# Optimization experiments

Measured on AMD Instinct MI355X. Metric: run time of the kernel, lower is better.

## Reference

```python
import jax, jax.numpy as jnp
import numpy as np
import math

D_MODEL = 1024
N_HEADS = 16
D_HEAD = D_MODEL // N_HEADS
D_FF = 4 * D_MODEL
EPS = 1e-5


def layer_norm(x, gamma, beta):
    mu = jnp.mean(x, axis=-1, keepdims=True)
    var = jnp.var(x, axis=-1, keepdims=True)
    return (x - mu) * jax.lax.rsqrt(var + EPS) * gamma + beta


def setup_inputs() -> dict:
    key = jax.random.key(0)
    ks = jax.random.split(key, 8)
    B, C, D = 32, 256, D_MODEL
    s = 0.02
    return {
        "X": jax.random.normal(ks[0], (B, C, D), dtype=jnp.float32),
        "W_qkv": jax.random.normal(ks[1], (D, 3 * D), dtype=jnp.float32) * s,
        "b_qkv": jnp.zeros((3 * D,), dtype=jnp.float32),
        "W_proj": jax.random.normal(ks[2], (D, D), dtype=jnp.float32) * s,
        "b_proj": jnp.zeros((D,), dtype=jnp.float32),
        "g1": jnp.ones((D,), dtype=jnp.float32),
        "beta1": jnp.zeros((D,), dtype=jnp.float32),
        "g2": jnp.ones((D,), dtype=jnp.float32),
        "beta2": jnp.zeros((D,), dtype=jnp.float32),
        "W_ff1": jax.random.normal(ks[3], (D, D_FF), dtype=jnp.float32) * s,
        "b_ff1": jnp.zeros((D_FF,), dtype=jnp.float32),
        "W_ff2": jax.random.normal(ks[4], (D_FF, D), dtype=jnp.float32) * s,
        "b_ff2": jnp.zeros((D,), dtype=jnp.float32),
    }


def reference(X, W_qkv, b_qkv, W_proj, b_proj, g1, beta1, g2, beta2,
              W_ff1, b_ff1, W_ff2, b_ff2):
    B, C, D = X.shape
    H, Dh = N_HEADS, D_HEAD
    scale = 1.0 / math.sqrt(Dh)

    Xn = layer_norm(X, g1, beta1)
    qkv = Xn @ W_qkv + b_qkv                       # [B, C, 3D]
    q, k, v = jnp.split(qkv, 3, axis=-1)
    # split heads -> [B, H, C, Dh]
    sh = lambda t: t.reshape(B, C, H, Dh).transpose(0, 2, 1, 3)
    q, k, v = sh(q), sh(k), sh(v)

    scores = jnp.einsum("bhcd,bhkd->bhck", q, k) * scale  # [B, H, C, C]
    attn = jax.nn.softmax(scores, axis=-1)
    ctx = jnp.einsum("bhck,bhkd->bhcd", attn, v)           # [B, H, C, Dh]
    ctx = ctx.transpose(0, 2, 1, 3).reshape(B, C, D)

    X1 = X + (ctx @ W_proj + b_proj)
    X2n = layer_norm(X1, g2, beta2)
    h = jax.nn.gelu(X2n @ W_ff1 + b_ff1, approximate=False)
    X_out = X1 + (h @ W_ff2 + b_ff2)
    A = attn.mean(axis=1)                                   # [B, C, C]
    return (X_out, A)
```

## Files before the change

### kernel.cpp

```cpp
#include <hip/hip_runtime.h>
#include <cstdint>
#include <cstddef>

typedef short bf16x8 __attribute__((ext_vector_type(8)));
typedef float f32x4 __attribute__((ext_vector_type(4)));
typedef unsigned short u16;
typedef u16 u16x8 __attribute__((ext_vector_type(8)));

#define GLD16(gptr, lptr)                                                            \
  __builtin_amdgcn_global_load_lds((const __attribute__((address_space(1))) void*)(gptr), \
                                   (__attribute__((address_space(3))) void*)(lptr), 16, 0, 0)

__device__ __forceinline__ u16 f2bf(float f) {
  union { float f; unsigned u; } v; v.f = f;
  unsigned r = v.u + 0x7FFF + ((v.u >> 16) & 1);
  return (u16)(r >> 16);
}
__device__ __forceinline__ float bf2f(u16 h) {
  union { unsigned u; float f; } v; v.u = ((unsigned)h) << 16;
  return v.f;
}

template <int N> __device__ __forceinline__ void vmwait() {
  if constexpr (N == 0) asm volatile("s_waitcnt vmcnt(0)" ::: "memory");
  else if constexpr (N == 6) asm volatile("s_waitcnt vmcnt(6)" ::: "memory");
  else asm volatile("s_waitcnt vmcnt(12)" ::: "memory");
}

__device__ __forceinline__ bf16x8 lds_read_sw64(const u16* base, int row, int col) {
  int byt = row * 128 + col * 2;
  byt ^= (row & 7) << 4;
  return *(const bf16x8*)((const char*)base + byt);
}

__global__ __launch_bounds__(256) void transpose_cast(const float* __restrict__ in,
                                                      u16* __restrict__ out, int R, int C) {
  __shared__ float tile[32][33];
  const int tx = threadIdx.x, ty = threadIdx.y;
  const int c0 = blockIdx.x * 32, r0 = blockIdx.y * 32;
#pragma unroll
  for (int i = 0; i < 32; i += 8)
    tile[ty + i][tx] = in[(size_t)(r0 + ty + i) * C + c0 + tx];
  __syncthreads();
#pragma unroll
  for (int i = 0; i < 32; i += 8)
    out[(size_t)(c0 + ty + i) * R + r0 + tx] = f2bf(tile[tx][ty + i]);
}

__global__ __launch_bounds__(256) void layernorm_bf16(const float* __restrict__ X,
                                                      const float* __restrict__ g,
                                                      const float* __restrict__ be,
                                                      u16* __restrict__ out) {
  const int row = blockIdx.x, t = threadIdx.x;
  const int lane = t & 63, wave = t >> 6;
  const float* x = X + (size_t)row * 1024;
  __shared__ float part[4];
  float v[4]; float s = 0.f;
#pragma unroll
  for (int i = 0; i < 4; ++i) { v[i] = x[t + i * 256]; s += v[i]; }
#pragma unroll
  for (int o = 32; o >= 1; o >>= 1) s += __shfl_xor(s, o);
  if (lane == 0) part[wave] = s;
  __syncthreads();
  const float mu = (part[0] + part[1] + part[2] + part[3]) * (1.f / 1024.f);
  float d2 = 0.f;
#pragma unroll
  for (int i = 0; i < 4; ++i) { float d = v[i] - mu; d2 += d * d; }
#pragma unroll
  for (int o = 32; o >= 1; o >>= 1) d2 += __shfl_xor(d2, o);
  __syncthreads();
  if (lane == 0) part[wave] = d2;
  __syncthreads();
  const float var = (part[0] + part[1] + part[2] + part[3]) * (1.f / 1024.f);
  const float rstd = rsqrtf(var + 1e-5f);
#pragma unroll
  for (int i = 0; i < 4; ++i) {
    const int c = t + i * 256;
    out[(size_t)row * 1024 + c] = f2bf((v[i] - mu) * rstd * g[c] + be[c]);
  }
}

template <int EPI>
__global__ __launch_bounds__(512, 1) void gemm_ring3(const u16* __restrict__ A,
                                                     const u16* __restrict__ Bt,
                                                     const float* __restrict__ bias,
                                                     const float* __restrict__ res,
                                                     float* __restrict__ outf,
                                                     u16* __restrict__ outb,
                                                     int M, int N, int K) {
  constexpr int ABYT = 256 * 128;
  constexpr int BBYT = 128 * 128;
  __shared__ __attribute__((aligned(16))) char lds[3 * (ABYT + BBYT)];

  const int t = threadIdx.x, lane = t & 63, wave = t >> 6;
  const int wm = wave >> 1, wn = wave & 1;
  const int l15 = lane & 15, l16 = lane >> 4;

  const int lb = (blockIdx.x & 7) * ((int)gridDim.x >> 3) + ((int)blockIdx.x >> 3);
  const int NBN = N >> 7;
  const int bm = (lb / NBN) * 256, bn = (lb % NBN) * 128;

  const u16* aptr[4];
  const u16* bptr[2];
#pragma unroll
  for (int c = 0; c < 4; ++c) {
    int Lb = c * 8192 + t * 16;
    int x = (Lb ^ ((Lb >> 3) & 0x70)) >> 1;
    aptr[c] = A + (size_t)(bm + (x >> 6)) * K + (x & 63);
  }
#pragma unroll
  for (int c = 0; c < 2; ++c) {
    int Lb = c * 8192 + t * 16;
    int x = (Lb ^ ((Lb >> 3) & 0x70)) >> 1;
    bptr[c] = Bt + (size_t)(bn + (x >> 6)) * K + (x & 63);
  }

  auto stage = [&](int p) {
    const int ko = p * 64;
    const int s = p % 3;
    char* ab = lds + s * ABYT + t * 16;
    char* bb = lds + 3 * ABYT + s * BBYT + t * 16;
#pragma unroll
    for (int c = 0; c < 4; ++c) GLD16(aptr[c] + ko, ab + c * 8192);
#pragma unroll
    for (int c = 0; c < 2; ++c) GLD16(bptr[c] + ko, bb + c * 8192);
  };
  stage(0); stage(1);

  const int rxA = ((wm * 64 + l15) & 7) << 4;
  const int co0 = l16 * 16, co1 = 64 + l16 * 16;

  f32x4 acc[4][4] = {};
  const int nkt = K >> 6;

#pragma unroll 1
  for (int kt = 0; kt < nkt; ++kt) {
    if (kt < nkt - 1) vmwait<6>(); else vmwait<0>();
    asm volatile("s_barrier" ::: "memory");
    if (kt + 2 < nkt) stage(kt + 2);

    const int s = kt % 3;
    const char* ab = lds + s * ABYT;
    const char* bb = lds + 3 * ABYT + s * BBYT;
    bf16x8 a[4][2], b[4][2];
#pragma unroll
    for (int m = 0; m < 4; ++m) {
      const int r = wm * 64 + m * 16 + l15;
      const int rb = r * 128, sw = (r & 7) << 4;
      a[m][0] = *(const bf16x8*)(ab + rb + (co0 ^ sw));
      a[m][1] = *(const bf16x8*)(ab + rb + (co1 ^ sw));
    }
#pragma unroll
    for (int n = 0; n < 4; ++n) {
      const int r = wn * 64 + n * 16 + l15;
      const int rb = r * 128, sw = (r & 7) << 4;
      b[n][0] = *(const bf16x8*)(bb + rb + (co0 ^ sw));
      b[n][1] = *(const bf16x8*)(bb + rb + (co1 ^ sw));
    }
    __builtin_amdgcn_s_setprio(1);
#pragma unroll
    for (int ks = 0; ks < 2; ++ks)
#pragma unroll
      for (int m = 0; m < 4; ++m)
#pragma unroll
        for (int n = 0; n < 4; ++n)
          acc[m][n] = __builtin_amdgcn_mfma_f32_16x16x32_bf16(a[m][ks], b[n][ks], acc[m][n], 0, 0, 0);
    __builtin_amdgcn_s_setprio(0);
  }

  const int r0 = l16 * 4;
#pragma unroll
  for (int m = 0; m < 4; ++m) {
#pragma unroll
    for (int n = 0; n < 4; ++n) {
      const int col = bn + wn * 64 + n * 16 + l15;
      const float bv = bias[col];
#pragma unroll
      for (int r = 0; r < 4; ++r) {
        const int row = bm + wm * 64 + m * 16 + r0 + r;
        const float v = acc[m][n][r] + bv;
        const size_t o = (size_t)row * N + col;
        if (EPI == 0) {
          outb[o] = f2bf(v);
        } else if (EPI == 1) {
          outf[o] = res[o] + v;
        } else {
          const float u = 0.7978845608f * (v + 0.044715f * v * v * v);
          const float e = __expf(2.f * u);
          const float th = 1.f - 2.f / (1.f + e);
          outb[o] = f2bf(0.5f * v * (1.f + th));
        }
      }
    }
  }
}

__global__ __launch_bounds__(256) void attn_scores(const u16* __restrict__ qkv,
                                                   u16* __restrict__ probs) {
  __shared__ u16 Ks[256 * 64];
  __shared__ u16 Qs[64 * 64];
  const int t = threadIdx.x, lane = t & 63, wave = t >> 6;
  const int qb = blockIdx.x * 64, h = blockIdx.y, b = blockIdx.z;
  const size_t row0 = (size_t)b * 256 * 3072;

#pragma unroll
  for (int is = 0; is < 8; ++is) {
    int L = (is * 2048 + t * 8) * 2;
    int x = (L ^ ((L >> 3) & 0x70)) >> 1;
    int kk = x >> 6, d = x & 63;
    const u16* gp = qkv + row0 + (size_t)kk * 3072 + 1024 + h * 64 + d;
    GLD16(gp, (char*)Ks + is * 4096 + wave * 1024);
  }
#pragma unroll
  for (int is = 0; is < 2; ++is) {
    int L = (is * 2048 + t * 8) * 2;
    int x = (L ^ ((L >> 3) & 0x70)) >> 1;
    int q = x >> 6, d = x & 63;
    const u16* gp = qkv + row0 + (size_t)(qb + q) * 3072 + h * 64 + d;
    GLD16(gp, (char*)Qs + is * 4096 + wave * 1024);
  }
  __syncthreads();

  f32x4 acc[16] = {};
  bf16x8 aq[2];
#pragma unroll
  for (int ks = 0; ks < 2; ++ks)
    aq[ks] = lds_read_sw64(Qs, wave * 16 + (lane & 15), ks * 32 + (lane >> 4) * 8);
#pragma unroll
  for (int nf = 0; nf < 16; ++nf) {
#pragma unroll
    for (int ks = 0; ks < 2; ++ks) {
      bf16x8 bk = lds_read_sw64(Ks, nf * 16 + (lane & 15), ks * 32 + (lane >> 4) * 8);
      acc[nf] = __builtin_amdgcn_mfma_f32_16x16x32_bf16(aq[ks], bk, acc[nf], 0, 0, 0);
    }
  }

  const int r0 = (lane >> 4) * 4, cc = lane & 15;
  const float sc = 0.125f;
#pragma unroll
  for (int r = 0; r < 4; ++r) {
    float mx = -1e30f;
#pragma unroll
    for (int nf = 0; nf < 16; ++nf) mx = fmaxf(mx, acc[nf][r]);
#pragma unroll
    for (int o = 8; o >= 1; o >>= 1) mx = fmaxf(mx, __shfl_xor(mx, o));
    float s = 0.f;
#pragma unroll
    for (int nf = 0; nf < 16; ++nf) {
      float e = __expf((acc[nf][r] - mx) * sc);
      acc[nf][r] = e; s += e;
    }
#pragma unroll
    for (int o = 8; o >= 1; o >>= 1) s += __shfl_xor(s, o);
    const float rinv = 1.f / s;
    const int qrow = qb + wave * 16 + r0 + r;
    u16* prow = probs + (size_t)((b * 16 + h) * 256 + qrow) * 256;
#pragma unroll
    for (int nf = 0; nf < 16; ++nf)
      prow[nf * 16 + cc] = f2bf(acc[nf][r] * rinv);
  }
}

__global__ __launch_bounds__(256) void amean(const u16* __restrict__ probs,
                                             float* __restrict__ A) {
  const int bq = blockIdx.x;
  const int b = bq >> 8, q = bq & 255;
  const int t = threadIdx.x;
  float s = 0.f;
#pragma unroll
  for (int h = 0; h < 16; ++h)
    s += bf2f(probs[(size_t)((b * 16 + h) * 256 + q) * 256 + t]);
  A[(size_t)bq * 256 + t] = s * (1.f / 16.f);
}

__global__ __launch_bounds__(256) void attn_pv(const u16* __restrict__ qkv,
                                               const u16* __restrict__ probs,
                                               u16* __restrict__ ctx) {
  __shared__ u16 Vs[64 * 256];
  const int t = threadIdx.x, lane = t & 63, wave = t >> 6;
  const int h = blockIdx.x, b = blockIdx.y;

#pragma unroll
  for (int p = 0; p < 8; ++p) {
    int idx = p * 2048 + t * 8;
    int kk = idx >> 6, d0 = idx & 63;
    u16x8 vv = *(const u16x8*)(qkv + (size_t)(b * 256 + kk) * 3072 + 2048 + h * 64 + d0);
#pragma unroll
    for (int j = 0; j < 8; ++j) {
      int d = d0 + j;
      int byt = (d * 512 + kk * 2) ^ ((d & 7) << 4);
      *(u16*)((char*)Vs + byt) = vv[j];
    }
  }
  __syncthreads();

  f32x4 acc[4][4] = {};
  const u16* Pb = probs + (size_t)((b * 16 + h) * 256) * 256;
  const int cc = lane & 15, kg = (lane >> 4) * 8;
#pragma unroll
  for (int kt = 0; kt < 8; ++kt) {
    bf16x8 a[4], v[4];
#pragma unroll
    for (int m = 0; m < 4; ++m)
      a[m] = *(const bf16x8*)(Pb + (size_t)(wave * 64 + m * 16 + cc) * 256 + kt * 32 + kg);
#pragma unroll
    for (int n = 0; n < 4; ++n) {
      int d = n * 16 + cc;
      int kk = kt * 32 + kg;
      int byt = (d * 512 + kk * 2) ^ ((d & 7) << 4);
      v[n] = *(const bf16x8*)((const char*)Vs + byt);
    }
#pragma unroll
    for (int m = 0; m < 4; ++m)
#pragma unroll
      for (int n = 0; n < 4; ++n)
        acc[m][n] = __builtin_amdgcn_mfma_f32_16x16x32_bf16(a[m], v[n], acc[m][n], 0, 0, 0);
  }

  const int r0 = (lane >> 4) * 4;
#pragma unroll
  for (int m = 0; m < 4; ++m) {
    const int q = wave * 64 + m * 16 + r0;
#pragma unroll
    for (int n = 0; n < 4; ++n) {
      const int col = h * 64 + n * 16 + cc;
#pragma unroll
      for (int r = 0; r < 4; ++r)
        ctx[(size_t)(b * 256 + q + r) * 1024 + col] = f2bf(acc[m][n][r]);
    }
  }
}

extern "C" void kernel_launch(void* const* d_in, const int* in_sizes, int n_in,
                              void* d_out, int out_size, void* d_ws, size_t ws_size,
                              hipStream_t stream) {
  const float* X      = (const float*)d_in[0];
  const float* W_qkv  = (const float*)d_in[1];
  const float* b_qkv  = (const float*)d_in[2];
  const float* W_proj = (const float*)d_in[3];
  const float* b_proj = (const float*)d_in[4];
  const float* g1     = (const float*)d_in[5];
  const float* beta1  = (const float*)d_in[6];
  const float* g2     = (const float*)d_in[7];
  const float* beta2  = (const float*)d_in[8];
  const float* W_ff1  = (const float*)d_in[9];
  const float* b_ff1  = (const float*)d_in[10];
  const float* W_ff2  = (const float*)d_in[11];
  const float* b_ff2  = (const float*)d_in[12];

  float* Xout = (float*)d_out;
  float* Aout = (float*)d_out + 8388608;

  char* ws = (char*)d_ws;
  const size_t MB = 1u << 20;
  u16* xn    = (u16*)(ws + 0);
  u16* wqkv  = (u16*)(ws + 16 * MB);
  u16* wproj = (u16*)(ws + 22 * MB);
  u16* wff1  = (u16*)(ws + 24 * MB);
  u16* wff2  = (u16*)(ws + 32 * MB);
  u16* qkv   = (u16*)(ws + 40 * MB);
  u16* probs = (u16*)(ws + 88 * MB);
  u16* hbuf  = probs;
  float* x1  = (float*)(ws + 152 * MB);
  u16* ctx   = xn;
  u16* x1n   = xn;

  const dim3 tb(32, 8);
  transpose_cast<<<dim3(96, 32),  tb, 0, stream>>>(W_qkv,  wqkv, 1024, 3072);
  transpose_cast<<<dim3(32, 32),  tb, 0, stream>>>(W_proj, wproj, 1024, 1024);
  transpose_cast<<<dim3(128, 32), tb, 0, stream>>>(W_ff1,  wff1, 1024, 4096);
  transpose_cast<<<dim3(32, 128), tb, 0, stream>>>(W_ff2,  wff2, 4096, 1024);

  layernorm_bf16<<<8192, 256, 0, stream>>>(X, g1, beta1, xn);

  gemm_ring3<0><<<768, 512, 0, stream>>>(xn, wqkv, b_qkv, nullptr, nullptr, qkv,
                                         8192, 3072, 1024);

  attn_scores<<<dim3(4, 16, 32), 256, 0, stream>>>(qkv, probs);
  amean<<<8192, 256, 0, stream>>>(probs, Aout);
  attn_pv<<<dim3(16, 32), 256, 0, stream>>>(qkv, probs, ctx);

  gemm_ring3<1><<<256, 512, 0, stream>>>(ctx, wproj, b_proj, X, x1, nullptr,
                                         8192, 1024, 1024);

  layernorm_bf16<<<8192, 256, 0, stream>>>(x1, g2, beta2, x1n);

  gemm_ring3<2><<<1024, 512, 0, stream>>>(x1n, wff1, b_ff1, nullptr, nullptr, hbuf,
                                          8192, 4096, 1024);

  gemm_ring3<1><<<256, 512, 0, stream>>>(hbuf, wff2, b_ff2, x1, Xout, nullptr,
                                         8192, 1024, 4096);
}
```

Baseline: 375.8 us.

## Replace triple-buffered GEMM with templated double-buffered kernel and larger N tiles

```diff
diff --git a/kernel.cpp b/kernel.cpp
--- a/kernel.cpp
+++ b/kernel.cpp
@@ -19,12 +19,6 @@
 __device__ __forceinline__ float bf2f(u16 h) {
   union { unsigned u; float f; } v; v.u = ((unsigned)h) << 16;
   return v.f;
-}
-
-template <int N> __device__ __forceinline__ void vmwait() {
-  if constexpr (N == 0) asm volatile("s_waitcnt vmcnt(0)" ::: "memory");
-  else if constexpr (N == 6) asm volatile("s_waitcnt vmcnt(6)" ::: "memory");
-  else asm volatile("s_waitcnt vmcnt(12)" ::: "memory");
 }
 
 __device__ __forceinline__ bf16x8 lds_read_sw64(const u16* base, int row, int col) {
@@ -80,36 +74,39 @@
   }
 }
 
-template <int EPI>
-__global__ __launch_bounds__(512, 1) void gemm_ring3(const u16* __restrict__ A,
-                                                     const u16* __restrict__ Bt,
-                                                     const float* __restrict__ bias,
-                                                     const float* __restrict__ res,
-                                                     float* __restrict__ outf,
-                                                     u16* __restrict__ outb,
-                                                     int M, int N, int K) {
-  constexpr int ABYT = 256 * 128;
-  constexpr int BBYT = 128 * 128;
-  __shared__ __attribute__((aligned(16))) char lds[3 * (ABYT + BBYT)];
+template <int EPI, int WM, int WN, int BN>
+__global__ __launch_bounds__(512, 2) void gemm_r2(const u16* __restrict__ A,
+                                                  const u16* __restrict__ Bt,
+                                                  const float* __restrict__ bias,
+                                                  const float* __restrict__ res,
+                                                  float* __restrict__ outf,
+                                                  u16* __restrict__ outb,
+                                                  int M, int N, int K) {
+  constexpr int BM = 256;
+  constexpr int WR = BM / WM, WC = BN / WN;
+  constexpr int MF = WR / 16, NF = WC / 16;
+  constexpr int ABYT = BM * 128, BBYT = BN * 128;
+  constexpr int LA = BM / 64, LB = BN / 64;
+  __shared__ __attribute__((aligned(16))) char lds[2 * (ABYT + BBYT)];
 
   const int t = threadIdx.x, lane = t & 63, wave = t >> 6;
-  const int wm = wave >> 1, wn = wave & 1;
+  const int wm = wave / WN, wn = wave % WN;
   const int l15 = lane & 15, l16 = lane >> 4;
 
   const int lb = (blockIdx.x & 7) * ((int)gridDim.x >> 3) + ((int)blockIdx.x >> 3);
-  const int NBN = N >> 7;
-  const int bm = (lb / NBN) * 256, bn = (lb % NBN) * 128;
-
-  const u16* aptr[4];
-  const u16* bptr[2];
-#pragma unroll
-  for (int c = 0; c < 4; ++c) {
+  const int NBN = N / BN;
+  const int bm = (lb / NBN) * BM, bn = (lb % NBN) * BN;
+
+  const u16* aptr[LA];
+  const u16* bptr[LB];
+#pragma unroll
+  for (int c = 0; c < LA; ++c) {
     int Lb = c * 8192 + t * 16;
     int x = (Lb ^ ((Lb >> 3) & 0x70)) >> 1;
     aptr[c] = A + (size_t)(bm + (x >> 6)) * K + (x & 63);
   }
 #pragma unroll
-  for (int c = 0; c < 2; ++c) {
+  for (int c = 0; c < LB; ++c) {
     int Lb = c * 8192 + t * 16;
     int x = (Lb ^ ((Lb >> 3) & 0x70)) >> 1;
     bptr[c] = Bt + (size_t)(bn + (x >> 6)) * K + (x & 63);
@@ -117,67 +114,64 @@
 
   auto stage = [&](int p) {
     const int ko = p * 64;
-    const int s = p % 3;
+    const int s = p & 1;
     char* ab = lds + s * ABYT + t * 16;
-    char* bb = lds + 3 * ABYT + s * BBYT + t * 16;
-#pragma unroll
-    for (int c = 0; c < 4; ++c) GLD16(aptr[c] + ko, ab + c * 8192);
-#pragma unroll
-    for (int c = 0; c < 2; ++c) GLD16(bptr[c] + ko, bb + c * 8192);
+    char* bb = lds + 2 * ABYT + s * BBYT + t * 16;
+#pragma unroll
+    for (int c = 0; c < LA; ++c) GLD16(aptr[c] + ko, ab + c * 8192);
+#pragma unroll
+    for (int c = 0; c < LB; ++c) GLD16(bptr[c] + ko, bb + c * 8192);
   };
-  stage(0); stage(1);
-
-  const int rxA = ((wm * 64 + l15) & 7) << 4;
+  stage(0);
+
   const int co0 = l16 * 16, co1 = 64 + l16 * 16;
-
-  f32x4 acc[4][4] = {};
+  f32x4 acc[MF][NF] = {};
   const int nkt = K >> 6;
 
 #pragma unroll 1
   for (int kt = 0; kt < nkt; ++kt) {
-    if (kt < nkt - 1) vmwait<6>(); else vmwait<0>();
+    asm volatile("s_waitcnt vmcnt(0)" ::: "memory");
+    asm volatile("s_waitcnt lgkmcnt(0)" ::: "memory");
     asm volatile("s_barrier" ::: "memory");
-    if (kt + 2 < nkt) stage(kt + 2);
-
-    const int s = kt % 3;
+    if (kt + 1 < nkt) stage(kt + 1);
+
+    const int s = kt & 1;
     const char* ab = lds + s * ABYT;
-    const char* bb = lds + 3 * ABYT + s * BBYT;
-    bf16x8 a[4][2], b[4][2];
-#pragma unroll
-    for (int m = 0; m < 4; ++m) {
-      const int r = wm * 64 + m * 16 + l15;
-      const int rb = r * 128, sw = (r & 7) << 4;
-      a[m][0] = *(const bf16x8*)(ab + rb + (co0 ^ sw));
-      a[m][1] = *(const bf16x8*)(ab + rb + (co1 ^ sw));
-    }
-#pragma unroll
-    for (int n = 0; n < 4; ++n) {
-      const int r = wn * 64 + n * 16 + l15;
-      const int rb = r * 128, sw = (r & 7) << 4;
-      b[n][0] = *(const bf16x8*)(bb + rb + (co0 ^ sw));
-      b[n][1] = *(const bf16x8*)(bb + rb + (co1 ^ sw));
-    }
-    __builtin_amdgcn_s_setprio(1);
-#pragma unroll
-    for (int ks = 0; ks < 2; ++ks)
-#pragma unroll
-      for (int m = 0; m < 4; ++m)
-#pragma unroll
-        for (int n = 0; n < 4; ++n)
-          acc[m][n] = __builtin_amdgcn_mfma_f32_16x16x32_bf16(a[m][ks], b[n][ks], acc[m][n], 0, 0, 0);
-    __builtin_amdgcn_s_setprio(0);
+    const char* bb = lds + 2 * ABYT + s * BBYT;
+#pragma unroll
+    for (int ks = 0; ks < 2; ++ks) {
+      const int co = ks ? co1 : co0;
+      bf16x8 a[MF], b[NF];
+#pragma unroll
+      for (int m = 0; m < MF; ++m) {
+        const int r = wm * WR + m * 16 + l15;
+        a[m] = *(const bf16x8*)(ab + r * 128 + (co ^ ((r & 7) << 4)));
+      }
+#pragma unroll
+      for (int n = 0; n < NF; ++n) {
+        const int r = wn * WC + n * 16 + l15;
+        b[n] = *(const bf16x8*)(bb + r * 128 + (co ^ ((r & 7) << 4)));
+      }
+      __builtin_amdgcn_s_setprio(1);
+#pragma unroll
+      for (int m = 0; m < MF; ++m)
+#pragma unroll
+        for (int n = 0; n < NF; ++n)
+          acc[m][n] = __builtin_amdgcn_mfma_f32_16x16x32_bf16(a[m], b[n], acc[m][n], 0, 0, 0);
+      __builtin_amdgcn_s_setprio(0);
+    }
   }
 
   const int r0 = l16 * 4;
 #pragma unroll
-  for (int m = 0; m < 4; ++m) {
-#pragma unroll
-    for (int n = 0; n < 4; ++n) {
-      const int col = bn + wn * 64 + n * 16 + l15;
+  for (int m = 0; m < MF; ++m) {
+#pragma unroll
+    for (int n = 0; n < NF; ++n) {
+      const int col = bn + wn * WC + n * 16 + l15;
       const float bv = bias[col];
 #pragma unroll
       for (int r = 0; r < 4; ++r) {
-        const int row = bm + wm * 64 + m * 16 + r0 + r;
+        const int row = bm + wm * WR + m * 16 + r0 + r;
         const float v = acc[m][n][r] + bv;
         const size_t o = (size_t)row * N + col;
         if (EPI == 0) {
@@ -373,21 +367,21 @@
 
   layernorm_bf16<<<8192, 256, 0, stream>>>(X, g1, beta1, xn);
 
-  gemm_ring3<0><<<768, 512, 0, stream>>>(xn, wqkv, b_qkv, nullptr, nullptr, qkv,
-                                         8192, 3072, 1024);
+  gemm_r2<0, 2, 4, 256><<<384, 512, 0, stream>>>(xn, wqkv, b_qkv, nullptr, nullptr, qkv,
+                                                 8192, 3072, 1024);
 
   attn_scores<<<dim3(4, 16, 32), 256, 0, stream>>>(qkv, probs);
   amean<<<8192, 256, 0, stream>>>(probs, Aout);
   attn_pv<<<dim3(16, 32), 256, 0, stream>>>(qkv, probs, ctx);
 
-  gemm_ring3<1><<<256, 512, 0, stream>>>(ctx, wproj, b_proj, X, x1, nullptr,
-                                         8192, 1024, 1024);
+  gemm_r2<1, 4, 2, 128><<<256, 512, 0, stream>>>(ctx, wproj, b_proj, X, x1, nullptr,
+                                                 8192, 1024, 1024);
 
   layernorm_bf16<<<8192, 256, 0, stream>>>(x1, g2, beta2, x1n);
 
-  gemm_ring3<2><<<1024, 512, 0, stream>>>(x1n, wff1, b_ff1, nullptr, nullptr, hbuf,
-                                          8192, 4096, 1024);
-
-  gemm_ring3<1><<<256, 512, 0, stream>>>(hbuf, wff2, b_ff2, x1, Xout, nullptr,
-                                         8192, 1024, 4096);
-}
+  gemm_r2<2, 2, 4, 256><<<512, 512, 0, stream>>>(x1n, wff1, b_ff1, nullptr, nullptr, hbuf,
+                                                 8192, 4096, 1024);
+
+  gemm_r2<1, 4, 2, 128><<<256, 512, 0, stream>>>(hbuf, wff2, b_ff2, x1, Xout, nullptr,
+                                                 8192, 1024, 4096);
+}
```

New measurement: 354.4 us. 1.06x faster.

## Replace 256x128 triple-buffered GEMM with 128x128 double-buffered tiles at two blocks/CU

Applied to the files above, without the earlier changes.

```diff
diff --git a/kernel.cpp b/kernel.cpp
--- a/kernel.cpp
+++ b/kernel.cpp
@@ -19,12 +19,6 @@
 __device__ __forceinline__ float bf2f(u16 h) {
   union { unsigned u; float f; } v; v.u = ((unsigned)h) << 16;
   return v.f;
-}
-
-template <int N> __device__ __forceinline__ void vmwait() {
-  if constexpr (N == 0) asm volatile("s_waitcnt vmcnt(0)" ::: "memory");
-  else if constexpr (N == 6) asm volatile("s_waitcnt vmcnt(6)" ::: "memory");
-  else asm volatile("s_waitcnt vmcnt(12)" ::: "memory");
 }
 
 __device__ __forceinline__ bf16x8 lds_read_sw64(const u16* base, int row, int col) {
@@ -81,91 +75,85 @@
 }
 
 template <int EPI>
-__global__ __launch_bounds__(512, 1) void gemm_ring3(const u16* __restrict__ A,
-                                                     const u16* __restrict__ Bt,
-                                                     const float* __restrict__ bias,
-                                                     const float* __restrict__ res,
-                                                     float* __restrict__ outf,
-                                                     u16* __restrict__ outb,
-                                                     int M, int N, int K) {
-  constexpr int ABYT = 256 * 128;
-  constexpr int BBYT = 128 * 128;
-  __shared__ __attribute__((aligned(16))) char lds[3 * (ABYT + BBYT)];
+__global__ __launch_bounds__(256, 2) void gemm_128(const u16* __restrict__ A,
+                                                   const u16* __restrict__ Bt,
+                                                   const float* __restrict__ bias,
+                                                   const float* __restrict__ res,
+                                                   float* __restrict__ outf,
+                                                   u16* __restrict__ outb,
+                                                   int M, int N, int K) {
+  constexpr int ABYT = 128 * 128;
+  __shared__ __attribute__((aligned(16))) char lds[4 * ABYT];
 
   const int t = threadIdx.x, lane = t & 63, wave = t >> 6;
   const int wm = wave >> 1, wn = wave & 1;
   const int l15 = lane & 15, l16 = lane >> 4;
 
-  const int lb = (blockIdx.x & 7) * ((int)gridDim.x >> 3) + ((int)blockIdx.x >> 3);
-  const int NBN = N >> 7;
-  const int bm = (lb / NBN) * 256, bn = (lb % NBN) * 128;
+  const int xcd = (int)blockIdx.x & 7, q = (int)blockIdx.x >> 3;
+  const int j = q & 63, gq = q >> 6;
+  const int g = gq * 8 + xcd;
+  const int NGN = N >> 10;
+  const int gm = g / NGN, gn = g % NGN;
+  const int bm = (gm * 8 + (j >> 3)) * 128;
+  const int bn = (gn * 8 + (j & 7)) * 128;
 
   const u16* aptr[4];
-  const u16* bptr[2];
+  const u16* bptr[4];
 #pragma unroll
   for (int c = 0; c < 4; ++c) {
-    int Lb = c * 8192 + t * 16;
+    int Lb = c * 4096 + t * 16;
     int x = (Lb ^ ((Lb >> 3) & 0x70)) >> 1;
     aptr[c] = A + (size_t)(bm + (x >> 6)) * K + (x & 63);
-  }
-#pragma unroll
-  for (int c = 0; c < 2; ++c) {
-    int Lb = c * 8192 + t * 16;
-    int x = (Lb ^ ((Lb >> 3) & 0x70)) >> 1;
     bptr[c] = Bt + (size_t)(bn + (x >> 6)) * K + (x & 63);
   }
 
   auto stage = [&](int p) {
     const int ko = p * 64;
-    const int s = p % 3;
+    const int s = p & 1;
     char* ab = lds + s * ABYT + t * 16;
-    char* bb = lds + 3 * ABYT + s * BBYT + t * 16;
-#pragma unroll
-    for (int c = 0; c < 4; ++c) GLD16(aptr[c] + ko, ab + c * 8192);
-#pragma unroll
-    for (int c = 0; c < 2; ++c) GLD16(bptr[c] + ko, bb + c * 8192);
+    char* bb = lds + 2 * ABYT + s * ABYT + t * 16;
+#pragma unroll
+    for (int c = 0; c < 4; ++c) GLD16(aptr[c] + ko, ab + c * 4096);
+#pragma unroll
+    for (int c = 0; c < 4; ++c) GLD16(bptr[c] + ko, bb + c * 4096);
   };
-  stage(0); stage(1);
-
-  const int rxA = ((wm * 64 + l15) & 7) << 4;
+  stage(0);
+
   const int co0 = l16 * 16, co1 = 64 + l16 * 16;
-
   f32x4 acc[4][4] = {};
   const int nkt = K >> 6;
 
 #pragma unroll 1
   for (int kt = 0; kt < nkt; ++kt) {
-    if (kt < nkt - 1) vmwait<6>(); else vmwait<0>();
+    asm volatile("s_waitcnt vmcnt(0)" ::: "memory");
     asm volatile("s_barrier" ::: "memory");
-    if (kt + 2 < nkt) stage(kt + 2);
-
-    const int s = kt % 3;
+    if (kt + 1 < nkt) stage(kt + 1);
+
+    const int s = kt & 1;
     const char* ab = lds + s * ABYT;
-    const char* bb = lds + 3 * ABYT + s * BBYT;
-    bf16x8 a[4][2], b[4][2];
-#pragma unroll
-    for (int m = 0; m < 4; ++m) {
-      const int r = wm * 64 + m * 16 + l15;
-      const int rb = r * 128, sw = (r & 7) << 4;
-      a[m][0] = *(const bf16x8*)(ab + rb + (co0 ^ sw));
-      a[m][1] = *(const bf16x8*)(ab + rb + (co1 ^ sw));
-    }
-#pragma unroll
-    for (int n = 0; n < 4; ++n) {
-      const int r = wn * 64 + n * 16 + l15;
-      const int rb = r * 128, sw = (r & 7) << 4;
-      b[n][0] = *(const bf16x8*)(bb + rb + (co0 ^ sw));
-      b[n][1] = *(const bf16x8*)(bb + rb + (co1 ^ sw));
-    }
-    __builtin_amdgcn_s_setprio(1);
-#pragma unroll
-    for (int ks = 0; ks < 2; ++ks)
+    const char* bb = lds + 2 * ABYT + s * ABYT;
+#pragma unroll
+    for (int ks = 0; ks < 2; ++ks) {
+      const int co = ks ? co1 : co0;
+      bf16x8 a[4], b[4];
+#pragma unroll
+      for (int m = 0; m < 4; ++m) {
+        const int r = wm * 64 + m * 16 + l15;
+        a[m] = *(const bf16x8*)(ab + r * 128 + (co ^ ((r & 7) << 4)));
+      }
+#pragma unroll
+      for (int n = 0; n < 4; ++n) {
+        const int r = wn * 64 + n * 16 + l15;
+        b[n] = *(const bf16x8*)(bb + r * 128 + (co ^ ((r & 7) << 4)));
+      }
+      __builtin_amdgcn_s_setprio(1);
 #pragma unroll
       for (int m = 0; m < 4; ++m)
 #pragma unroll
         for (int n = 0; n < 4; ++n)
-          acc[m][n] = __builtin_amdgcn_mfma_f32_16x16x32_bf16(a[m][ks], b[n][ks], acc[m][n], 0, 0, 0);
-    __builtin_amdgcn_s_setprio(0);
+          acc[m][n] = __builtin_amdgcn_mfma_f32_16x16x32_bf16(a[m], b[n], acc[m][n], 0, 0, 0);
+      __builtin_amdgcn_s_setprio(0);
+    }
   }
 
   const int r0 = l16 * 4;
@@ -373,21 +361,21 @@
 
   layernorm_bf16<<<8192, 256, 0, stream>>>(X, g1, beta1, xn);
 
-  gemm_ring3<0><<<768, 512, 0, stream>>>(xn, wqkv, b_qkv, nullptr, nullptr, qkv,
-                                         8192, 3072, 1024);
+  gemm_128<0><<<1536, 256, 0, stream>>>(xn, wqkv, b_qkv, nullptr, nullptr, qkv,
+                                        8192, 3072, 1024);
 
   attn_scores<<<dim3(4, 16, 32), 256, 0, stream>>>(qkv, probs);
   amean<<<8192, 256, 0, stream>>>(probs, Aout);
   attn_pv<<<dim3(16, 32), 256, 0, stream>>>(qkv, probs, ctx);
 
-  gemm_ring3<1><<<256, 512, 0, stream>>>(ctx, wproj, b_proj, X, x1, nullptr,
-                                         8192, 1024, 1024);
+  gemm_128<1><<<512, 256, 0, stream>>>(ctx, wproj, b_proj, X, x1, nullptr,
+                                       8192, 1024, 1024);
 
   layernorm_bf16<<<8192, 256, 0, stream>>>(x1, g2, beta2, x1n);
 
-  gemm_ring3<2><<<1024, 512, 0, stream>>>(x1n, wff1, b_ff1, nullptr, nullptr, hbuf,
-                                          8192, 4096, 1024);
-
-  gemm_ring3<1><<<256, 512, 0, stream>>>(hbuf, wff2, b_ff2, x1, Xout, nullptr,
-                                         8192, 1024, 4096);
-}
+  gemm_128<2><<<2048, 256, 0, stream>>>(x1n, wff1, b_ff1, nullptr, nullptr, hbuf,
+                                        8192, 4096, 1024);
+
+  gemm_128<1><<<512, 256, 0, stream>>>(hbuf, wff2, b_ff2, x1, Xout, nullptr,
+                                       8192, 1024, 4096);
+}
```

After: 336.7 us. -10.4%, faster.
